# Performance work log

Measured on AMD Instinct MI355X. Metric: run time of the kernel, lower is better.

## Reference

```python
import jax, jax.numpy as jnp
import numpy as np

B, N, IN_DIM, OUT_DIM, H = 4, 2048, 128, 128, 4
NEG_SLOPE = 0.2


def setup_inputs() -> dict:
    key = jax.random.key(0)
    ks = jax.random.split(key, 6)
    # Xavier-ish scaling for stable softmax logits
    node_features = jax.random.normal(ks[0], (B, N, IN_DIM), dtype=jnp.float32)
    adjacency = jax.random.randint(ks[1], (B, N, N), 0, 2, dtype=jnp.int32)
    W = jax.random.normal(ks[2], (H, IN_DIM, OUT_DIM), dtype=jnp.float32) / np.sqrt(IN_DIM)
    a = jax.random.normal(ks[3], (H, 2 * OUT_DIM), dtype=jnp.float32) / np.sqrt(2 * OUT_DIM)
    out_proj_w = jax.random.normal(ks[4], (H * OUT_DIM, OUT_DIM), dtype=jnp.float32) / np.sqrt(H * OUT_DIM)
    out_proj_b = jax.random.normal(ks[5], (OUT_DIM,), dtype=jnp.float32) * 0.01
    return {"node_features": node_features, "adjacency": adjacency, "W": W,
            "a": a, "out_proj_w": out_proj_w, "out_proj_b": out_proj_b}


def reference(node_features, adjacency, W, a, out_proj_w, out_proj_b):
    D = W.shape[-1]
    # Per-head projection: h[b,h,n,o]
    h = jnp.einsum('bni,hio->bhno', node_features, W)
    # Additive attention score a^T [h_i || h_j] decomposed into src+dst parts
    # (exact since the score Linear has no bias).
    s = jnp.einsum('bhno,ho->bhn', h, a[:, :D])   # contribution of h_i
    d = jnp.einsum('bhno,ho->bhn', h, a[:, D:])   # contribution of h_j
    e = jax.nn.leaky_relu(s[..., :, None] + d[..., None, :], NEG_SLOPE)  # [B,H,N,N]
    e = jnp.where(adjacency[:, None, :, :] == 0, -jnp.inf, e)
    alpha = jax.nn.softmax(e, axis=-1)                                   # [B,H,N,N]
    out = jnp.einsum('bhnm,bhmo->bhno', alpha, h)                        # [B,H,N,D]
    b, nh, n, _ = out.shape
    cat = out.transpose(0, 2, 1, 3).reshape(b, n, nh * D)                # concat heads
    output = cat @ out_proj_w + out_proj_b                               # [B,N,D]
    return output, alpha
```

## Files before the change

kernel.cpp:

```cpp
#include <hip/hip_runtime.h>
#include <hip/hip_bf16.h>

#define BB 4
#define NN 2048
#define DD 128
#define HH 4
#define LOG2E 1.4426950408889634f
#define NEG_BIG (-1e30f)

typedef __attribute__((ext_vector_type(8))) short bf16x8;
typedef __attribute__((ext_vector_type(4))) short bf16x4;
typedef __attribute__((ext_vector_type(4))) float f32x4;

__device__ __forceinline__ unsigned short f2bf(float f) {
    union { float f; unsigned int u; } v; v.f = f;
    unsigned int r = v.u + 0x7FFF + ((v.u >> 16) & 1);
    return (unsigned short)(r >> 16);
}

__global__ __launch_bounds__(128) void k_wvec(const float* __restrict__ W,
                                              const float* __restrict__ a,
                                              float* __restrict__ wsv,
                                              float* __restrict__ wdv) {
    int h = blockIdx.x;
    int i = threadIdx.x;
    const float* Wr  = W + (h * DD + i) * DD;
    const float* as_ = a + h * 2 * DD;
    const float* ad_ = as_ + DD;
    float s = 0.f, d = 0.f;
    for (int o = 0; o < DD; ++o) {
        float w = Wr[o];
        s += w * as_[o];
        d += w * ad_[o];
    }
    wsv[h * DD + i] = s;
    wdv[h * DD + i] = d;
}

__global__ __launch_bounds__(256) void k_sd(const float* __restrict__ x,
                                            const float* __restrict__ wsv,
                                            const float* __restrict__ wdv,
                                            float* __restrict__ s_out,
                                            float* __restrict__ d_out_) {
    __shared__ float xs[64 * 129];
    __shared__ float ws[4 * 129], wd[4 * 129];
    int tid = threadIdx.x;
    int b  = blockIdx.x / (NN / 64);
    int nb = (blockIdx.x % (NN / 64)) * 64;
    for (int idx = tid; idx < HH * DD; idx += 256) {
        ws[(idx >> 7) * 129 + (idx & 127)] = wsv[idx];
        wd[(idx >> 7) * 129 + (idx & 127)] = wdv[idx];
    }
    for (int idx = tid; idx < 64 * 128; idx += 256) {
        int r = idx >> 7, c = idx & 127;
        xs[r * 129 + c] = x[((size_t)b * NN + nb + r) * DD + c];
    }
    __syncthreads();
    int h = tid & 3, r = tid >> 2;
    float sv = 0.f, dv = 0.f;
#pragma unroll 8
    for (int i = 0; i < DD; ++i) {
        float xv = xs[r * 129 + i];
        sv += xv * ws[h * 129 + i];
        dv += xv * wd[h * 129 + i];
    }
    int n = nb + r;
    s_out[(b * HH + h) * NN + n] = sv;
    d_out_[(b * HH + h) * NN + n] = dv;
}

__global__ __launch_bounds__(256) void k_h(const float* __restrict__ x,
                                           const float* __restrict__ W,
                                           unsigned short* __restrict__ hT) {
    __shared__ float xs[32 * 132];
    int tid = threadIdx.x;
    int bh = blockIdx.x / (NN / 32);
    int nb = (blockIdx.x % (NN / 32)) * 32;
    int b = bh >> 2, h = bh & 3;
    for (int idx = tid; idx < 32 * 128; idx += 256) {
        int r = idx >> 7, c = idx & 127;
        xs[r * 132 + c] = x[((size_t)b * NN + nb + r) * DD + c];
    }
    __syncthreads();
    int o = tid & 127, rh = tid >> 7;
    float acc[16];
#pragma unroll
    for (int j = 0; j < 16; ++j) acc[j] = 0.f;
    const float* Wc = W + (size_t)h * DD * DD + o;
    for (int i = 0; i < DD; i += 4) {
        float w0 = Wc[(i + 0) * DD];
        float w1 = Wc[(i + 1) * DD];
        float w2 = Wc[(i + 2) * DD];
        float w3 = Wc[(i + 3) * DD];
#pragma unroll
        for (int j = 0; j < 16; ++j) {
            float4 xq = *(const float4*)&xs[(rh * 16 + j) * 132 + i];
            acc[j] += xq.x * w0 + xq.y * w1 + xq.z * w2 + xq.w * w3;
        }
    }
    bf16x8 p0, p1;
#pragma unroll
    for (int j = 0; j < 8; ++j) { p0[j] = (short)f2bf(acc[j]); p1[j] = (short)f2bf(acc[8 + j]); }
    unsigned short* dst = hT + ((size_t)bh * DD + o) * NN + nb + rh * 16;
    *(bf16x8*)dst = p0;
    *(bf16x8*)(dst + 8) = p1;
}

__global__ __launch_bounds__(256) void k_stats(const int* __restrict__ adj,
                                               const float* __restrict__ s_in,
                                               const float* __restrict__ d_in_,
                                               float* __restrict__ M_out,
                                               float* __restrict__ Li_out) {
    __shared__ float part[4][4];
    int tid = threadIdx.x;
    int lane = tid & 63, w = tid >> 6;
    int b = blockIdx.x / NN, n = blockIdx.x % NN;
    const int* arow = adj + ((size_t)b * NN + n) * NN;
    int av[8];
#pragma unroll
    for (int k = 0; k < 8; ++k) av[k] = arow[tid + k * 256];
    float dv[8][4];
#pragma unroll
    for (int h = 0; h < 4; ++h) {
        const float* dp = d_in_ + (size_t)(b * HH + h) * NN;
#pragma unroll
        for (int k = 0; k < 8; ++k) dv[k][h] = dp[tid + k * 256];
    }
    float sv[4];
#pragma unroll
    for (int h = 0; h < 4; ++h) sv[h] = s_in[(b * HH + h) * NN + n];

    float mx[4];
#pragma unroll
    for (int h = 0; h < 4; ++h) mx[h] = NEG_BIG;
#pragma unroll
    for (int k = 0; k < 8; ++k)
#pragma unroll
        for (int h = 0; h < 4; ++h)
            mx[h] = (av[k] != 0 && dv[k][h] > mx[h]) ? dv[k][h] : mx[h];
#pragma unroll
    for (int off = 32; off >= 1; off >>= 1)
#pragma unroll
        for (int h = 0; h < 4; ++h)
            mx[h] = fmaxf(mx[h], __shfl_xor(mx[h], off, 64));
    if (lane == 0)
#pragma unroll
        for (int h = 0; h < 4; ++h) part[h][w] = mx[h];
    __syncthreads();
    float M[4];
#pragma unroll
    for (int h = 0; h < 4; ++h) {
        float md = fmaxf(fmaxf(part[h][0], part[h][1]), fmaxf(part[h][2], part[h][3]));
        float t = sv[h] + md;
        M[h] = t > 0.f ? t : 0.2f * t;
    }
    __syncthreads();

    float L[4] = {0.f, 0.f, 0.f, 0.f};
#pragma unroll
    for (int k = 0; k < 8; ++k)
#pragma unroll
        for (int h = 0; h < 4; ++h) {
            float t = sv[h] + dv[k][h];
            float v = t > 0.f ? t : 0.2f * t;
            float e = exp2f((v - M[h]) * LOG2E);
            L[h] += (av[k] != 0) ? e : 0.f;
        }
#pragma unroll
    for (int off = 32; off >= 1; off >>= 1)
#pragma unroll
        for (int h = 0; h < 4; ++h)
            L[h] += __shfl_xor(L[h], off, 64);
    if (lane == 0)
#pragma unroll
        for (int h = 0; h < 4; ++h) part[h][w] = L[h];
    __syncthreads();
    if (tid == 0) {
#pragma unroll
        for (int h = 0; h < 4; ++h) {
            float Lt = part[h][0] + part[h][1] + part[h][2] + part[h][3];
            M_out[(b * HH + h) * NN + n]  = M[h];
            Li_out[(b * HH + h) * NN + n] = Lt > 0.f ? 1.f / Lt : 0.f;
        }
    }
}

template <bool WRITE_ALPHA>
__global__ __launch_bounds__(256) void k_attn_mfma(const int* __restrict__ adj,
                                                   const float* __restrict__ s_in,
                                                   const float* __restrict__ d_in_,
                                                   const float* __restrict__ M_in,
                                                   const float* __restrict__ Li_in,
                                                   const unsigned short* __restrict__ hT,
                                                   float* __restrict__ out_scr,
                                                   float* __restrict__ alpha_out) {
    __shared__ unsigned short al_lds[64 * 128];
    __shared__ unsigned short hT_lds[128 * 128];
    __shared__ float srow[64], Mrow[64], Lirow[64];
    int tid = threadIdx.x;
    int bh = blockIdx.x >> 5;
    int nb = (blockIdx.x & 31) * 64;
    int b = bh >> 2;

    if (tid < 64) {
        srow[tid]  = s_in[bh * NN + nb + tid];
        Mrow[tid]  = M_in[bh * NN + nb + tid];
        Lirow[tid] = Li_in[bh * NN + nb + tid];
    }

    int ar0 = tid >> 5;
    int ac4 = (tid & 31) * 4;
    const int* adj_base = adj + ((size_t)b * NN + nb + ar0) * NN + ac4;
    float* alpha_base = WRITE_ALPHA
        ? alpha_out + ((size_t)bh * NN + nb + ar0) * NN + ac4 : nullptr;
    const float* dg = d_in_ + (size_t)bh * NN;
    int ho = tid >> 1, hhalf = (tid & 1) * 64;
    const unsigned short* hrow = hT + ((size_t)bh * DD + ho) * NN;
    int l = tid & 63, w = tid >> 6, col = l & 15, quad = l >> 4;

    f32x4 acc[8];
#pragma unroll
    for (int ot = 0; ot < 8; ++ot) acc[ot] = (f32x4){0.f, 0.f, 0.f, 0.f};

    for (int mb = 0; mb < NN; mb += 128) {
        __syncthreads();

        int4 a4[8];
#pragma unroll
        for (int p = 0; p < 8; ++p)
            a4[p] = *(const int4*)(adj_base + (size_t)(p * 8) * NN + mb);
        float4 d4 = *(const float4*)(dg + mb + ac4);
        bf16x8 hv[8];
#pragma unroll
        for (int q = 0; q < 8; ++q)
            hv[q] = *(const bf16x8*)(hrow + mb + hhalf + q * 8);

#pragma unroll
        for (int p = 0; p < 8; ++p) {
            int row = p * 8 + ar0;
            float sn = srow[row], Mn = Mrow[row], Lin = Lirow[row];
            float t0 = sn + d4.x, t1 = sn + d4.y, t2 = sn + d4.z, t3 = sn + d4.w;
            float v0 = t0 > 0.f ? t0 : 0.2f * t0;
            float v1 = t1 > 0.f ? t1 : 0.2f * t1;
            float v2 = t2 > 0.f ? t2 : 0.2f * t2;
            float v3 = t3 > 0.f ? t3 : 0.2f * t3;
            float e0 = (a4[p].x != 0) ? exp2f((v0 - Mn) * LOG2E) * Lin : 0.f;
            float e1 = (a4[p].y != 0) ? exp2f((v1 - Mn) * LOG2E) * Lin : 0.f;
            float e2 = (a4[p].z != 0) ? exp2f((v2 - Mn) * LOG2E) * Lin : 0.f;
            float e3 = (a4[p].w != 0) ? exp2f((v3 - Mn) * LOG2E) * Lin : 0.f;
            bf16x4 pk;
            pk[0] = (short)f2bf(e0); pk[1] = (short)f2bf(e1);
            pk[2] = (short)f2bf(e2); pk[3] = (short)f2bf(e3);
            int abyte = (ac4 * 2) ^ ((row & 15) << 4);
            *(bf16x4*)&al_lds[row * 128 + (abyte >> 1)] = pk;
            if (WRITE_ALPHA) {
                float4 ev; ev.x = e0; ev.y = e1; ev.z = e2; ev.w = e3;
                *(float4*)(alpha_base + (size_t)(p * 8) * NN + mb) = ev;
            }
        }
#pragma unroll
        for (int q = 0; q < 8; ++q) {
            int hbyte = (hhalf * 2 + q * 16) ^ ((ho & 15) << 4);
            *(bf16x8*)&hT_lds[ho * 128 + (hbyte >> 1)] = hv[q];
        }
        __syncthreads();
#pragma unroll
        for (int k = 0; k < 4; ++k) {
            int cbyte = (k * 64 + quad * 16) ^ (col << 4);
            bf16x8 af = *(const bf16x8*)&al_lds[(w * 16 + col) * 128 + (cbyte >> 1)];
#pragma unroll
            for (int ot = 0; ot < 8; ++ot) {
                bf16x8 bfv = *(const bf16x8*)&hT_lds[(ot * 16 + col) * 128 + (cbyte >> 1)];
                acc[ot] = __builtin_amdgcn_mfma_f32_16x16x32_bf16(af, bfv, acc[ot], 0, 0, 0);
            }
        }
    }
#pragma unroll
    for (int ot = 0; ot < 8; ++ot)
#pragma unroll
        for (int r = 0; r < 4; ++r)
            out_scr[((size_t)bh * NN + nb + w * 16 + quad * 4 + r) * DD + ot * 16 + col] =
                acc[ot][r];
}

__global__ __launch_bounds__(256) void k_proj(const float* __restrict__ out_scr,
                                              const float* __restrict__ Wp,
                                              const float* __restrict__ bias,
                                              float* __restrict__ out) {
    __shared__ float cs[16 * 512];
    int tid = threadIdx.x;
    int b  = blockIdx.x / (NN / 16);
    int nb = (blockIdx.x % (NN / 16)) * 16;
    for (int idx = tid; idx < 16 * 512; idx += 256) {
        int r = idx >> 9, c = idx & 511;
        int hh = c >> 7, oo = c & 127;
        cs[idx] = out_scr[((size_t)(b * HH + hh) * NN + nb + r) * DD + oo];
    }
    __syncthreads();
    int o = tid & 63, rg = tid >> 6;
    float bv0 = bias[o], bv1 = bias[o + 64];
    float acc0[4], acc1[4];
#pragma unroll
    for (int j = 0; j < 4; ++j) { acc0[j] = bv0; acc1[j] = bv1; }
    for (int k = 0; k < 512; k += 4) {
        float w00 = Wp[(k + 0) * DD + o], w01 = Wp[(k + 0) * DD + o + 64];
        float w10 = Wp[(k + 1) * DD + o], w11 = Wp[(k + 1) * DD + o + 64];
        float w20 = Wp[(k + 2) * DD + o], w21 = Wp[(k + 2) * DD + o + 64];
        float w30 = Wp[(k + 3) * DD + o], w31 = Wp[(k + 3) * DD + o + 64];
#pragma unroll
        for (int j = 0; j < 4; ++j) {
            float4 cq = *(const float4*)&cs[(rg * 4 + j) * 512 + k];
            acc0[j] += cq.x * w00 + cq.y * w10 + cq.z * w20 + cq.w * w30;
            acc1[j] += cq.x * w01 + cq.y * w11 + cq.z * w21 + cq.w * w31;
        }
    }
#pragma unroll
    for (int j = 0; j < 4; ++j) {
        out[((size_t)b * NN + nb + rg * 4 + j) * DD + o]      = acc0[j];
        out[((size_t)b * NN + nb + rg * 4 + j) * DD + o + 64] = acc1[j];
    }
}

__global__ __launch_bounds__(256) void k_alpha(const int* __restrict__ adj,
                                               const float* __restrict__ s_in,
                                               const float* __restrict__ d_in_,
                                               const float* __restrict__ M_in,
                                               const float* __restrict__ Li_in,
                                               float* __restrict__ alpha_out) {
    int tid = threadIdx.x;
    int b = blockIdx.x / NN, n = blockIdx.x % NN;
    float sv[4], Mv[4], Lv[4];
#pragma unroll
    for (int h = 0; h < 4; ++h) {
        sv[h] = s_in[(b * HH + h) * NN + n];
        Mv[h] = M_in[(b * HH + h) * NN + n];
        Lv[h] = Li_in[(b * HH + h) * NN + n];
    }
    const int* arow = adj + ((size_t)b * NN + n) * NN;
    for (int m = tid; m < NN; m += 256) {
        int av = arow[m];
#pragma unroll
        for (int h = 0; h < 4; ++h) {
            float val = 0.f;
            if (av != 0) {
                float t = sv[h] + d_in_[(b * HH + h) * NN + m];
                float v = t > 0.f ? t : 0.2f * t;
                val = exp2f((v - Mv[h]) * LOG2E) * Lv[h];
            }
            alpha_out[((size_t)(b * HH + h) * NN + n) * NN + m] = val;
        }
    }
}

extern "C" void kernel_launch(void* const* d_in, const int* in_sizes, int n_in,
                              void* d_out, int out_size, void* d_ws, size_t ws_size,
                              hipStream_t stream) {
    const float* x    = (const float*)d_in[0];
    const int*   adj  = (const int*)d_in[1];
    const float* W    = (const float*)d_in[2];
    const float* a    = (const float*)d_in[3];
    const float* Wp   = (const float*)d_in[4];
    const float* bias = (const float*)d_in[5];

    float* out       = (float*)d_out;
    float* alpha_out = out + (size_t)BB * NN * DD;

    float* ws  = (float*)d_ws;
    float* wsv = ws;
    float* wdv = wsv + HH * DD;
    float* s_  = wdv + HH * DD;
    float* d_  = s_ + (size_t)BB * HH * NN;
    float* M_  = d_ + (size_t)BB * HH * NN;
    float* Li_ = M_ + (size_t)BB * HH * NN;

    const size_t stats_bytes = (2 * HH * DD + 4 * (size_t)BB * HH * NN) * sizeof(float);
    const size_t hT_bytes    = (size_t)BB * HH * NN * DD * sizeof(unsigned short);
    const size_t scr_bytes   = (size_t)BB * HH * NN * DD * sizeof(float);
    const bool fused = ws_size >= stats_bytes + hT_bytes + scr_bytes;

    unsigned short* hT;
    float* out_scr;
    if (fused) {
        hT      = (unsigned short*)((char*)d_ws + stats_bytes);
        out_scr = (float*)((char*)hT + hT_bytes);
    } else {
        hT      = (unsigned short*)alpha_out;
        out_scr = alpha_out + (size_t)BB * HH * NN * DD;
    }

    k_wvec<<<HH, 128, 0, stream>>>(W, a, wsv, wdv);
    k_sd<<<BB * NN / 64, 256, 0, stream>>>(x, wsv, wdv, s_, d_);
    k_h<<<BB * HH * (NN / 32), 256, 0, stream>>>(x, W, hT);
    k_stats<<<BB * NN, 256, 0, stream>>>(adj, s_, d_, M_, Li_);
    if (fused) {
        k_attn_mfma<true><<<BB * HH * (NN / 64), 256, 0, stream>>>(adj, s_, d_, M_, Li_,
                                                                   hT, out_scr, alpha_out);
        k_proj<<<BB * (NN / 16), 256, 0, stream>>>(out_scr, Wp, bias, out);
    } else {
        k_attn_mfma<false><<<BB * HH * (NN / 64), 256, 0, stream>>>(adj, s_, d_, M_, Li_,
                                                                    hT, out_scr, alpha_out);
        k_proj<<<BB * (NN / 16), 256, 0, stream>>>(out_scr, Wp, bias, out);
        k_alpha<<<BB * NN, 256, 0, stream>>>(adj, s_, d_, M_, Li_, alpha_out);
    }
}
```

Before: 469.8 us.

## Prefetch next attention tile into registers, fuse s/d into k_h, remap blocks

The attention kernel now double-buffers global loads of adjacency, d and hT in registers. The next tile is loaded while the current tile's softmax weights and MFMA products are computed, which hides memory latency. The s/d score projection is folded into the k_h kernel, removing one launch and a second read of x. The hT load pattern and the block-to-tile mapping are also changed so that neighbouring blocks are spread across batch-heads. In exchange, register pressure rises from holding two tile buffers, and the last iteration issues one redundant wrap-around load.

```diff
diff --git a/kernel.cpp b/kernel.cpp
--- a/kernel.cpp
+++ b/kernel.cpp
@@ -37,41 +37,13 @@
     wdv[h * DD + i] = d;
 }
 
-__global__ __launch_bounds__(256) void k_sd(const float* __restrict__ x,
-                                            const float* __restrict__ wsv,
-                                            const float* __restrict__ wdv,
-                                            float* __restrict__ s_out,
-                                            float* __restrict__ d_out_) {
-    __shared__ float xs[64 * 129];
-    __shared__ float ws[4 * 129], wd[4 * 129];
-    int tid = threadIdx.x;
-    int b  = blockIdx.x / (NN / 64);
-    int nb = (blockIdx.x % (NN / 64)) * 64;
-    for (int idx = tid; idx < HH * DD; idx += 256) {
-        ws[(idx >> 7) * 129 + (idx & 127)] = wsv[idx];
-        wd[(idx >> 7) * 129 + (idx & 127)] = wdv[idx];
-    }
-    for (int idx = tid; idx < 64 * 128; idx += 256) {
-        int r = idx >> 7, c = idx & 127;
-        xs[r * 129 + c] = x[((size_t)b * NN + nb + r) * DD + c];
-    }
-    __syncthreads();
-    int h = tid & 3, r = tid >> 2;
-    float sv = 0.f, dv = 0.f;
-#pragma unroll 8
-    for (int i = 0; i < DD; ++i) {
-        float xv = xs[r * 129 + i];
-        sv += xv * ws[h * 129 + i];
-        dv += xv * wd[h * 129 + i];
-    }
-    int n = nb + r;
-    s_out[(b * HH + h) * NN + n] = sv;
-    d_out_[(b * HH + h) * NN + n] = dv;
-}
-
 __global__ __launch_bounds__(256) void k_h(const float* __restrict__ x,
                                            const float* __restrict__ W,
-                                           unsigned short* __restrict__ hT) {
+                                           const float* __restrict__ wsv,
+                                           const float* __restrict__ wdv,
+                                           unsigned short* __restrict__ hT,
+                                           float* __restrict__ s_out,
+                                           float* __restrict__ d_out_) {
     __shared__ float xs[32 * 132];
     int tid = threadIdx.x;
     int bh = blockIdx.x / (NN / 32);
@@ -104,6 +76,30 @@
     unsigned short* dst = hT + ((size_t)bh * DD + o) * NN + nb + rh * 16;
     *(bf16x8*)dst = p0;
     *(bf16x8*)(dst + 8) = p1;
+
+    {
+        int r = tid >> 3, seg = (tid & 7) * 16;
+        const float* wsp = wsv + h * DD + seg;
+        const float* wdp = wdv + h * DD + seg;
+        float sv = 0.f, dv = 0.f;
+#pragma unroll
+        for (int j = 0; j < 16; j += 4) {
+            float4 xq = *(const float4*)&xs[r * 132 + seg + j];
+            float4 wq = *(const float4*)(wsp + j);
+            float4 vq = *(const float4*)(wdp + j);
+            sv += xq.x * wq.x + xq.y * wq.y + xq.z * wq.z + xq.w * wq.w;
+            dv += xq.x * vq.x + xq.y * vq.y + xq.z * vq.z + xq.w * vq.w;
+        }
+#pragma unroll
+        for (int off = 1; off < 8; off <<= 1) {
+            sv += __shfl_xor(sv, off, 64);
+            dv += __shfl_xor(dv, off, 64);
+        }
+        if ((tid & 7) == 0) {
+            s_out[(b * HH + h) * NN + nb + r]  = sv;
+            d_out_[(b * HH + h) * NN + nb + r] = dv;
+        }
+    }
 }
 
 __global__ __launch_bounds__(256) void k_stats(const int* __restrict__ adj,
@@ -183,6 +179,79 @@
             Li_out[(b * HH + h) * NN + n] = Lt > 0.f ? 1.f / Lt : 0.f;
         }
     }
+}
+
+struct TileRegs {
+    int4   a4[8];
+    float4 d4;
+    bf16x8 hv[8];
+};
+
+__device__ __forceinline__ void attn_load_tile(int mb, const int* adj_base,
+                                               const float* dg, int ac4,
+                                               const unsigned short* hbase,
+                                               TileRegs& R) {
+#pragma unroll
+    for (int p = 0; p < 8; ++p)
+        R.a4[p] = *(const int4*)(adj_base + (size_t)(p * 8) * NN + mb);
+    R.d4 = *(const float4*)(dg + mb + ac4);
+#pragma unroll
+    for (int q = 0; q < 8; ++q)
+        R.hv[q] = *(const bf16x8*)(hbase + (size_t)(q * 16) * NN + mb);
+}
+
+template <bool WRITE_ALPHA>
+__device__ __forceinline__ void attn_tile_body(
+    int mb, TileRegs& cur, TileRegs& nxt,
+    const int* adj_base, const float* dg, int ac4,
+    const unsigned short* hbase,
+    unsigned short* al_lds, unsigned short* hT_lds,
+    const float* srow, const float* Mrow, const float* Lirow,
+    float* alpha_base, int ar0, int hrow0, int hbyte,
+    int w, int col, int quad, f32x4 (&acc)[8])
+{
+#pragma unroll
+    for (int p = 0; p < 8; ++p) {
+        int row = p * 8 + ar0;
+        float sn = srow[row], Mn = Mrow[row], Lin = Lirow[row];
+        float t0 = sn + cur.d4.x, t1 = sn + cur.d4.y;
+        float t2 = sn + cur.d4.z, t3 = sn + cur.d4.w;
+        float v0 = t0 > 0.f ? t0 : 0.2f * t0;
+        float v1 = t1 > 0.f ? t1 : 0.2f * t1;
+        float v2 = t2 > 0.f ? t2 : 0.2f * t2;
+        float v3 = t3 > 0.f ? t3 : 0.2f * t3;
+        float e0 = (cur.a4[p].x != 0) ? exp2f((v0 - Mn) * LOG2E) * Lin : 0.f;
+        float e1 = (cur.a4[p].y != 0) ? exp2f((v1 - Mn) * LOG2E) * Lin : 0.f;
+        float e2 = (cur.a4[p].z != 0) ? exp2f((v2 - Mn) * LOG2E) * Lin : 0.f;
+        float e3 = (cur.a4[p].w != 0) ? exp2f((v3 - Mn) * LOG2E) * Lin : 0.f;
+        bf16x4 pk;
+        pk[0] = (short)f2bf(e0); pk[1] = (short)f2bf(e1);
+        pk[2] = (short)f2bf(e2); pk[3] = (short)f2bf(e3);
+        int abyte = (ac4 * 2) ^ ((row & 15) << 4);
+        *(bf16x4*)&al_lds[row * 128 + (abyte >> 1)] = pk;
+        if (WRITE_ALPHA) {
+            float4 ev; ev.x = e0; ev.y = e1; ev.z = e2; ev.w = e3;
+            *(float4*)(alpha_base + (size_t)(p * 8) * NN + mb) = ev;
+        }
+    }
+#pragma unroll
+    for (int q = 0; q < 8; ++q)
+        *(bf16x8*)&hT_lds[(q * 16 + hrow0) * 128 + (hbyte >> 1)] = cur.hv[q];
+
+    attn_load_tile((mb + 128) & (NN - 1), adj_base, dg, ac4, hbase, nxt);
+
+    __syncthreads();
+#pragma unroll
+    for (int k = 0; k < 4; ++k) {
+        int cbyte = (k * 64 + quad * 16) ^ (col << 4);
+        bf16x8 af = *(const bf16x8*)&al_lds[(w * 16 + col) * 128 + (cbyte >> 1)];
+#pragma unroll
+        for (int ot = 0; ot < 8; ++ot) {
+            bf16x8 bfv = *(const bf16x8*)&hT_lds[(ot * 16 + col) * 128 + (cbyte >> 1)];
+            acc[ot] = __builtin_amdgcn_mfma_f32_16x16x32_bf16(af, bfv, acc[ot], 0, 0, 0);
+        }
+    }
+    __syncthreads();
 }
 
 template <bool WRITE_ALPHA>
@@ -198,8 +267,9 @@
     __shared__ unsigned short hT_lds[128 * 128];
     __shared__ float srow[64], Mrow[64], Lirow[64];
     int tid = threadIdx.x;
-    int bh = blockIdx.x >> 5;
-    int nb = (blockIdx.x & 31) * 64;
+    int bid = (int)(blockIdx.x & 7) * 64 + (int)(blockIdx.x >> 3);
+    int bh = bid >> 5;
+    int nb = (bid & 31) * 64;
     int b = bh >> 2;
 
     if (tid < 64) {
@@ -214,66 +284,29 @@
     float* alpha_base = WRITE_ALPHA
         ? alpha_out + ((size_t)bh * NN + nb + ar0) * NN + ac4 : nullptr;
     const float* dg = d_in_ + (size_t)bh * NN;
-    int ho = tid >> 1, hhalf = (tid & 1) * 64;
-    const unsigned short* hrow = hT + ((size_t)bh * DD + ho) * NN;
+    int hrow0 = tid >> 4;
+    int hcolu = (tid & 15) * 8;
+    const unsigned short* hbase = hT + ((size_t)bh * DD + hrow0) * NN + hcolu;
+    int hbyte = (hcolu * 2) ^ (hrow0 << 4);
     int l = tid & 63, w = tid >> 6, col = l & 15, quad = l >> 4;
 
     f32x4 acc[8];
 #pragma unroll
     for (int ot = 0; ot < 8; ++ot) acc[ot] = (f32x4){0.f, 0.f, 0.f, 0.f};
 
-    for (int mb = 0; mb < NN; mb += 128) {
-        __syncthreads();
-
-        int4 a4[8];
-#pragma unroll
-        for (int p = 0; p < 8; ++p)
-            a4[p] = *(const int4*)(adj_base + (size_t)(p * 8) * NN + mb);
-        float4 d4 = *(const float4*)(dg + mb + ac4);
-        bf16x8 hv[8];
-#pragma unroll
-        for (int q = 0; q < 8; ++q)
-            hv[q] = *(const bf16x8*)(hrow + mb + hhalf + q * 8);
-
-#pragma unroll
-        for (int p = 0; p < 8; ++p) {
-            int row = p * 8 + ar0;
-            float sn = srow[row], Mn = Mrow[row], Lin = Lirow[row];
-            float t0 = sn + d4.x, t1 = sn + d4.y, t2 = sn + d4.z, t3 = sn + d4.w;
-            float v0 = t0 > 0.f ? t0 : 0.2f * t0;
-            float v1 = t1 > 0.f ? t1 : 0.2f * t1;
-            float v2 = t2 > 0.f ? t2 : 0.2f * t2;
-            float v3 = t3 > 0.f ? t3 : 0.2f * t3;
-            float e0 = (a4[p].x != 0) ? exp2f((v0 - Mn) * LOG2E) * Lin : 0.f;
-            float e1 = (a4[p].y != 0) ? exp2f((v1 - Mn) * LOG2E) * Lin : 0.f;
-            float e2 = (a4[p].z != 0) ? exp2f((v2 - Mn) * LOG2E) * Lin : 0.f;
-            float e3 = (a4[p].w != 0) ? exp2f((v3 - Mn) * LOG2E) * Lin : 0.f;
-            bf16x4 pk;
-            pk[0] = (short)f2bf(e0); pk[1] = (short)f2bf(e1);
-            pk[2] = (short)f2bf(e2); pk[3] = (short)f2bf(e3);
-            int abyte = (ac4 * 2) ^ ((row & 15) << 4);
-            *(bf16x4*)&al_lds[row * 128 + (abyte >> 1)] = pk;
-            if (WRITE_ALPHA) {
-                float4 ev; ev.x = e0; ev.y = e1; ev.z = e2; ev.w = e3;
-                *(float4*)(alpha_base + (size_t)(p * 8) * NN + mb) = ev;
-            }
-        }
-#pragma unroll
-        for (int q = 0; q < 8; ++q) {
-            int hbyte = (hhalf * 2 + q * 16) ^ ((ho & 15) << 4);
-            *(bf16x8*)&hT_lds[ho * 128 + (hbyte >> 1)] = hv[q];
-        }
-        __syncthreads();
-#pragma unroll
-        for (int k = 0; k < 4; ++k) {
-            int cbyte = (k * 64 + quad * 16) ^ (col << 4);
-            bf16x8 af = *(const bf16x8*)&al_lds[(w * 16 + col) * 128 + (cbyte >> 1)];
-#pragma unroll
-            for (int ot = 0; ot < 8; ++ot) {
-                bf16x8 bfv = *(const bf16x8*)&hT_lds[(ot * 16 + col) * 128 + (cbyte >> 1)];
-                acc[ot] = __builtin_amdgcn_mfma_f32_16x16x32_bf16(af, bfv, acc[ot], 0, 0, 0);
-            }
-        }
+    TileRegs R0, R1;
+    attn_load_tile(0, adj_base, dg, ac4, hbase, R0);
+    __syncthreads();
+
+    for (int mb = 0; mb < NN; mb += 256) {
+        attn_tile_body<WRITE_ALPHA>(mb, R0, R1, adj_base, dg, ac4, hbase,
+                                    al_lds, hT_lds, srow, Mrow, Lirow,
+                                    alpha_base, ar0, hrow0, hbyte,
+                                    w, col, quad, acc);
+        attn_tile_body<WRITE_ALPHA>(mb + 128, R1, R0, adj_base, dg, ac4, hbase,
+                                    al_lds, hT_lds, srow, Mrow, Lirow,
+                                    alpha_base, ar0, hrow0, hbyte,
+                                    w, col, quad, acc);
     }
 #pragma unroll
     for (int ot = 0; ot < 8; ++ot)
@@ -389,8 +422,7 @@
     }
 
     k_wvec<<<HH, 128, 0, stream>>>(W, a, wsv, wdv);
-    k_sd<<<BB * NN / 64, 256, 0, stream>>>(x, wsv, wdv, s_, d_);
-    k_h<<<BB * HH * (NN / 32), 256, 0, stream>>>(x, W, hT);
+    k_h<<<BB * HH * (NN / 32), 256, 0, stream>>>(x, W, wsv, wdv, hT, s_, d_);
     k_stats<<<BB * NN, 256, 0, stream>>>(adj, s_, d_, M_, Li_);
     if (fused) {
         k_attn_mfma<true><<<BB * HH * (NN / 64), 256, 0, stream>>>(adj, s_, d_, M_, Li_,
```

After: 454.9 us. -3.2%, faster.
